# Kernel optimization log

Measured on AMD Instinct MI355X. Metric: run time of the kernel, lower is better.

Reference implementation:

```python
import jax, jax.numpy as jnp
import numpy as np

EPS = 1e-12  # tf.nn.l2_normalize epsilon


def setup_inputs() -> dict:
    key = jax.random.key(0)
    k1, k2, k3 = jax.random.split(key, 3)
    T, NC, FW = 16384, 2048, 100
    x = jax.random.normal(k1, (T, NC), dtype=jnp.float32)
    weights = jax.random.normal(k2, (FW, NC), dtype=jnp.float32)
    biases = jax.random.normal(k3, (1, NC), dtype=jnp.float32)
    return {"x": x, "weights": weights, "biases": biases}


def reference(x, weights, biases):
    # x: [T, NC] (batch_size is the time axis), weights: [FW, NC], biases: [1, NC]
    FW, NC = weights.shape
    # pos_constraint then L2-normalize each filter along the lag axis
    w = jnp.maximum(weights, 0.0)
    w = w * jax.lax.rsqrt(jnp.maximum(jnp.sum(w * w, axis=0, keepdims=True), EPS))
    # The original pads the filter with FW trailing zeros and runs a SAME conv2d
    # over a [NC, T, 1, 1] input, then takes diag_part to recover the per-channel
    # result. With kernel size 2*FW, SAME pads (FW-1) above / FW below; the FW
    # trailing zero taps never contribute, so this equals a cross-correlation
    # with left padding FW-1: out[t, c] = sum_k w[k, c] * x[t + k - (FW-1), c].
    xT = x.T[None]                 # [1, NC, T]
    kern = w.T[:, None, :]         # [NC, 1, FW] depthwise kernel (OIH)
    pre = jax.lax.conv_general_dilated(
        xT, kern,
        window_strides=(1,),
        padding=[(FW - 1, 0)],
        dimension_numbers=("NCH", "OIH", "NCH"),
        feature_group_count=NC,
    )                              # [1, NC, T]
    pre = pre[0].T + biases        # [T, NC]
    return pre  # activation_func='lin' -> identity
```

## Files before the change

### kernel.cpp

```cpp
#include <hip/hip_runtime.h>


#define T_TOT 16384
#define NCH   2048
#define FW    100
#define CB    32
#define TB    128
#define NTHR  256
#define ROWL  292
#define NSEG  8
#define NCHUNK (T_TOT / TB / NSEG)

#define KC_STEP(KI, PH, NS) do {                                                \
    int ro_ = (base0 + (KI)*8 + 16) & 255;                                      \
    float4 n0_ = *(const float4*)(rrow + ro_);                                  \
    float4 n1_ = *(const float4*)(rrow + ro_ + 4);                              \
    xw[(NS)+0]=n0_.x; xw[(NS)+1]=n0_.y; xw[(NS)+2]=n0_.z; xw[(NS)+3]=n0_.w;     \
    xw[(NS)+4]=n1_.x; xw[(NS)+5]=n1_.y; xw[(NS)+6]=n1_.z; xw[(NS)+7]=n1_.w;     \
    _Pragma("unroll")                                                           \
    for (int u_ = 0; u_ < 8; ++u_) {                                            \
      _Pragma("unroll")                                                         \
      for (int i_ = 0; i_ < 16; ++i_)                                           \
        acc[i_] = fmaf(wreg[(KI)*8 + u_], xw[((PH) + u_ + i_) % 24], acc[i_]);  \
    }                                                                           \
} while (0)

__global__ __launch_bounds__(NTHR, 2)
void catent_fir(const float* __restrict__ x,
                const float* __restrict__ wraw,
                const float* __restrict__ bias,
                float* __restrict__ out) {
    __shared__ __align__(16) float ring[CB * ROWL];

    const int tid   = threadIdx.x;
    const int cgrp  = blockIdx.x & 63;
    const int sidx  = blockIdx.x >> 6;
    const int cbase = cgrp * CB;

    const int ch0 = sidx * NCHUNK;
    const int tseg0 = ch0 * TB;

    const int c = tid & 31;
    const int g = tid >> 5;

    float wreg[104];
    {
        const float* wcol = wraw + cbase + c;
        float s = 0.0f;
        wreg[0] = 0.0f;
        #pragma unroll
        for (int j = 1; j <= FW; ++j) {
            float v = fmaxf(wcol[(size_t)(j - 1) * NCH], 0.0f);
            wreg[j] = v;
            s = fmaf(v, v, s);
        }
        wreg[101] = 0.0f; wreg[102] = 0.0f; wreg[103] = 0.0f;
        float scl = rsqrtf(fmaxf(s, 1e-12f));
        #pragma unroll
        for (int j = 1; j <= FW; ++j) wreg[j] *= scl;
    }

    {
        float* rw = &ring[c * ROWL];
        for (int p = 0; p < 2; ++p) {
            int tbase = tseg0 - TB + p * TB + g * 16;
            float v[16];
            #pragma unroll
            for (int j = 0; j < 16; ++j) {
                int t = tbase + j;
                v[j] = (t >= 0) ? x[(size_t)t * NCH + cbase + c] : 0.0f;
            }
            int rm = tbase & 255;
            #pragma unroll
            for (int q = 0; q < 4; ++q)
                *(float4*)(rw + rm + q * 4) = make_float4(v[q*4], v[q*4+1], v[q*4+2], v[q*4+3]);
            if (rm < 32) {
                #pragma unroll
                for (int q = 0; q < 4; ++q)
                    *(float4*)(rw + 256 + rm + q * 4) = make_float4(v[q*4], v[q*4+1], v[q*4+2], v[q*4+3]);
            }
        }
    }
    __syncthreads();

    const float biasr = bias[cbase + c];
    const float* rrow = &ring[c * ROWL];
    float* rwr = &ring[c * ROWL];

    for (int ch = ch0; ch < ch0 + NCHUNK; ++ch) {
        const int t0 = ch * TB;
        const bool do_stage = (ch + 1 < ch0 + NCHUNK);

        float stv[16];
        if (do_stage) {
            const size_t gb = (size_t)(t0 + TB + g * 16) * NCH + cbase + c;
            #pragma unroll
            for (int j = 0; j < 16; ++j) stv[j] = x[gb + (size_t)j * NCH];
        }

        float acc[16];
        #pragma unroll
        for (int i = 0; i < 16; ++i) acc[i] = biasr;

        float xw[24];
        const int base0 = t0 + g * 16 - 100;

        {
            int ro = base0 & 255;
            #pragma unroll
            for (int q = 0; q < 6; ++q) {
                float4 v = *(const float4*)(rrow + ro + q * 4);
                xw[q*4+0] = v.x; xw[q*4+1] = v.y; xw[q*4+2] = v.z; xw[q*4+3] = v.w;
            }
            #pragma unroll
            for (int u = 0; u < 8; ++u) {
                #pragma unroll
                for (int i = 0; i < 16; ++i)
                    acc[i] = fmaf(wreg[u], xw[(u + i) % 24], acc[i]);
            }
        }

        KC_STEP(1,  8, 0);
        KC_STEP(2, 16, 8);
        KC_STEP(3,  0, 16);
        KC_STEP(4,  8, 0);
        KC_STEP(5, 16, 8);
        KC_STEP(6,  0, 16);
        KC_STEP(7,  8, 0);
        KC_STEP(8, 16, 8);
        KC_STEP(9,  0, 16);
        KC_STEP(10, 8, 0);
        KC_STEP(11,16, 8);
        KC_STEP(12, 0, 16);

        __syncthreads();

        if (do_stage) {
            int rm = (t0 + TB + g * 16) & 255;
            #pragma unroll
            for (int q = 0; q < 4; ++q)
                *(float4*)(rwr + rm + q * 4) = make_float4(stv[q*4], stv[q*4+1], stv[q*4+2], stv[q*4+3]);
            if (rm < 32) {
                #pragma unroll
                for (int q = 0; q < 4; ++q)
                    *(float4*)(rwr + 256 + rm + q * 4) = make_float4(stv[q*4], stv[q*4+1], stv[q*4+2], stv[q*4+3]);
            }
        }
        __syncthreads();

        {
            size_t ob = (size_t)(t0 + g * 16) * NCH + cbase + c;
            #pragma unroll
            for (int i = 0; i < 16; ++i) out[ob + (size_t)i * NCH] = acc[i];
        }
    }
}

extern "C" void kernel_launch(void* const* d_in, const int* in_sizes, int n_in,
                              void* d_out, int out_size, void* d_ws, size_t ws_size,
                              hipStream_t stream) {
    const float* x    = (const float*)d_in[0];
    const float* wraw = (const float*)d_in[1];
    const float* bias = (const float*)d_in[2];
    float* out = (float*)d_out;

    dim3 grid(64 * NSEG);
    dim3 block(NTHR);
    catent_fir<<<grid, block, 0, stream>>>(x, wraw, bias, out);
}
```

Before: 107.1 us.

## Move normalized filter taps from registers to LDS to raise occupancy

The 104 per-thread weight registers are replaced by a per-channel weight table in shared memory, written by the first warp group and read back as float4 pairs inside each KC step. Launch bounds go from 2 to 3 blocks per SM, and the time axis is split into 12 uneven segments instead of 8 so the grid is larger. This aims to cut register pressure and raise occupancy and latency hiding, at the cost of extra LDS reads per chunk and more halo reloads across segments. There is no barrier between the LDS weight writes and the first reads, but the existing __syncthreads after ring staging already covers this.

Result: slower. 321.0 us (+199.8%).

```diff
diff --git a/kernel.cpp b/kernel.cpp
--- a/kernel.cpp
+++ b/kernel.cpp
@@ -8,56 +8,69 @@
 #define TB    128
 #define NTHR  256
 #define ROWL  292
-#define NSEG  8
-#define NCHUNK (T_TOT / TB / NSEG)
+#define WROW  108
+#define NSEG  12
+#define NCHUNK_TOT (T_TOT / TB)
 
 #define KC_STEP(KI, PH, NS) do {                                                \
     int ro_ = (base0 + (KI)*8 + 16) & 255;                                      \
     float4 n0_ = *(const float4*)(rrow + ro_);                                  \
     float4 n1_ = *(const float4*)(rrow + ro_ + 4);                              \
+    float4 w0_ = *(const float4*)(wrow + (KI)*8);                               \
+    float4 w1_ = *(const float4*)(wrow + (KI)*8 + 4);                           \
     xw[(NS)+0]=n0_.x; xw[(NS)+1]=n0_.y; xw[(NS)+2]=n0_.z; xw[(NS)+3]=n0_.w;     \
     xw[(NS)+4]=n1_.x; xw[(NS)+5]=n1_.y; xw[(NS)+6]=n1_.z; xw[(NS)+7]=n1_.w;     \
+    float wk_[8];                                                               \
+    wk_[0]=w0_.x; wk_[1]=w0_.y; wk_[2]=w0_.z; wk_[3]=w0_.w;                     \
+    wk_[4]=w1_.x; wk_[5]=w1_.y; wk_[6]=w1_.z; wk_[7]=w1_.w;                     \
     _Pragma("unroll")                                                           \
     for (int u_ = 0; u_ < 8; ++u_) {                                            \
       _Pragma("unroll")                                                         \
       for (int i_ = 0; i_ < 16; ++i_)                                           \
-        acc[i_] = fmaf(wreg[(KI)*8 + u_], xw[((PH) + u_ + i_) % 24], acc[i_]);  \
+        acc[i_] = fmaf(wk_[u_], xw[((PH) + u_ + i_) % 24], acc[i_]);            \
     }                                                                           \
 } while (0)
 
-__global__ __launch_bounds__(NTHR, 2)
+__global__ __launch_bounds__(NTHR, 3)
 void catent_fir(const float* __restrict__ x,
                 const float* __restrict__ wraw,
                 const float* __restrict__ bias,
                 float* __restrict__ out) {
     __shared__ __align__(16) float ring[CB * ROWL];
+    __shared__ __align__(16) float wl[CB * WROW];
 
     const int tid   = threadIdx.x;
     const int cgrp  = blockIdx.x & 63;
     const int sidx  = blockIdx.x >> 6;
     const int cbase = cgrp * CB;
 
-    const int ch0 = sidx * NCHUNK;
+    const int ch0 = (sidx * NCHUNK_TOT) / NSEG;
+    const int ch1 = ((sidx + 1) * NCHUNK_TOT) / NSEG;
     const int tseg0 = ch0 * TB;
 
     const int c = tid & 31;
     const int g = tid >> 5;
 
-    float wreg[104];
     {
         const float* wcol = wraw + cbase + c;
+        float wt[104];
         float s = 0.0f;
-        wreg[0] = 0.0f;
+        wt[0] = 0.0f;
         #pragma unroll
         for (int j = 1; j <= FW; ++j) {
             float v = fmaxf(wcol[(size_t)(j - 1) * NCH], 0.0f);
-            wreg[j] = v;
+            wt[j] = v;
             s = fmaf(v, v, s);
         }
-        wreg[101] = 0.0f; wreg[102] = 0.0f; wreg[103] = 0.0f;
+        wt[101] = 0.0f; wt[102] = 0.0f; wt[103] = 0.0f;
         float scl = rsqrtf(fmaxf(s, 1e-12f));
-        #pragma unroll
-        for (int j = 1; j <= FW; ++j) wreg[j] *= scl;
+        if (g == 0) {
+            float* wr = &wl[c * WROW];
+            #pragma unroll
+            for (int q = 0; q < 26; ++q)
+                *(float4*)(wr + q * 4) = make_float4(wt[q*4] * scl, wt[q*4+1] * scl,
+                                                    wt[q*4+2] * scl, wt[q*4+3] * scl);
+        }
     }
 
     {
@@ -85,11 +98,12 @@
 
     const float biasr = bias[cbase + c];
     const float* rrow = &ring[c * ROWL];
+    const float* wrow = &wl[c * WROW];
     float* rwr = &ring[c * ROWL];
 
-    for (int ch = ch0; ch < ch0 + NCHUNK; ++ch) {
+    for (int ch = ch0; ch < ch1; ++ch) {
         const int t0 = ch * TB;
-        const bool do_stage = (ch + 1 < ch0 + NCHUNK);
+        const bool do_stage = (ch + 1 < ch1);
 
         float stv[16];
         if (do_stage) {
@@ -112,11 +126,16 @@
                 float4 v = *(const float4*)(rrow + ro + q * 4);
                 xw[q*4+0] = v.x; xw[q*4+1] = v.y; xw[q*4+2] = v.z; xw[q*4+3] = v.w;
             }
+            float4 w0 = *(const float4*)(wrow);
+            float4 w1 = *(const float4*)(wrow + 4);
+            float wk[8];
+            wk[0]=w0.x; wk[1]=w0.y; wk[2]=w0.z; wk[3]=w0.w;
+            wk[4]=w1.x; wk[5]=w1.y; wk[6]=w1.z; wk[7]=w1.w;
             #pragma unroll
             for (int u = 0; u < 8; ++u) {
                 #pragma unroll
                 for (int i = 0; i < 16; ++i)
-                    acc[i] = fmaf(wreg[u], xw[(u + i) % 24], acc[i]);
+                    acc[i] = fmaf(wk[u], xw[(u + i) % 24], acc[i]);
             }
         }
 
```

## Precompute normalized weights in a prep kernel and stream them from global memory

Applied to the files above, without the earlier changes.

Adds a small prep kernel that applies the ReLU and L2 normalization and writes per-channel transposed weights into a global buffer. The main FIR kernel drops its 104-register weight array and instead loads 8 weights at a time via double-buffered float4 loads. The prefetch of the next x chunk is moved from before the compute to after the barrier, which cuts register pressure but removes the overlap between the global loads and the FMAs. The goals are lower VGPR usage and higher occupancy, at the cost of repeated weight loads from cache each chunk and a second kernel launch.

Result: slower. 123.6 us (+15.4%).

```diff
diff --git a/kernel.cpp b/kernel.cpp
--- a/kernel.cpp
+++ b/kernel.cpp
@@ -8,26 +8,51 @@
 #define TB    128
 #define NTHR  256
 #define ROWL  292
+#define WTL   104
 #define NSEG  8
 #define NCHUNK (T_TOT / TB / NSEG)
 
-#define KC_STEP(KI, PH, NS) do {                                                \
+__device__ float g_wT[NCH * WTL];
+
+__global__ void prep_w(const float* __restrict__ wraw) {
+    int c = blockIdx.x * 256 + threadIdx.x;
+    const float* wcol = wraw + c;
+    float s = 0.0f;
+    for (int k = 0; k < FW; ++k) {
+        float v = fmaxf(wcol[(size_t)k * NCH], 0.0f);
+        s = fmaf(v, v, s);
+    }
+    float scl = rsqrtf(fmaxf(s, 1e-12f));
+    float* wr = g_wT + (size_t)c * WTL;
+    wr[0] = 0.0f;
+    for (int j = 1; j <= FW; ++j)
+        wr[j] = fmaxf(wcol[(size_t)(j - 1) * NCH], 0.0f) * scl;
+    wr[101] = 0.0f; wr[102] = 0.0f; wr[103] = 0.0f;
+}
+
+#define KC_STEP(KI, PH, NS, WB0, WB1, DOLD, LDOFF) do {                         \
     int ro_ = (base0 + (KI)*8 + 16) & 255;                                      \
     float4 n0_ = *(const float4*)(rrow + ro_);                                  \
     float4 n1_ = *(const float4*)(rrow + ro_ + 4);                              \
+    float wk_[8];                                                               \
+    wk_[0]=WB0.x; wk_[1]=WB0.y; wk_[2]=WB0.z; wk_[3]=WB0.w;                     \
+    wk_[4]=WB1.x; wk_[5]=WB1.y; wk_[6]=WB1.z; wk_[7]=WB1.w;                     \
+    if (DOLD) {                                                                 \
+        WB0 = *(const float4*)(wrow + (LDOFF));                                 \
+        WB1 = *(const float4*)(wrow + (LDOFF) + 4);                             \
+    }                                                                           \
     xw[(NS)+0]=n0_.x; xw[(NS)+1]=n0_.y; xw[(NS)+2]=n0_.z; xw[(NS)+3]=n0_.w;     \
     xw[(NS)+4]=n1_.x; xw[(NS)+5]=n1_.y; xw[(NS)+6]=n1_.z; xw[(NS)+7]=n1_.w;     \
     _Pragma("unroll")                                                           \
     for (int u_ = 0; u_ < 8; ++u_) {                                            \
       _Pragma("unroll")                                                         \
       for (int i_ = 0; i_ < 16; ++i_)                                           \
-        acc[i_] = fmaf(wreg[(KI)*8 + u_], xw[((PH) + u_ + i_) % 24], acc[i_]);  \
+        acc[i_] = fmaf(wk_[u_], xw[((PH) + u_ + i_) % 24], acc[i_]);            \
     }                                                                           \
 } while (0)
 
 __global__ __launch_bounds__(NTHR, 2)
 void catent_fir(const float* __restrict__ x,
-                const float* __restrict__ wraw,
                 const float* __restrict__ bias,
                 float* __restrict__ out) {
     __shared__ __align__(16) float ring[CB * ROWL];
@@ -42,23 +67,6 @@
 
     const int c = tid & 31;
     const int g = tid >> 5;
-
-    float wreg[104];
-    {
-        const float* wcol = wraw + cbase + c;
-        float s = 0.0f;
-        wreg[0] = 0.0f;
-        #pragma unroll
-        for (int j = 1; j <= FW; ++j) {
-            float v = fmaxf(wcol[(size_t)(j - 1) * NCH], 0.0f);
-            wreg[j] = v;
-            s = fmaf(v, v, s);
-        }
-        wreg[101] = 0.0f; wreg[102] = 0.0f; wreg[103] = 0.0f;
-        float scl = rsqrtf(fmaxf(s, 1e-12f));
-        #pragma unroll
-        for (int j = 1; j <= FW; ++j) wreg[j] *= scl;
-    }
 
     {
         float* rw = &ring[c * ROWL];
@@ -85,18 +93,17 @@
 
     const float biasr = bias[cbase + c];
     const float* rrow = &ring[c * ROWL];
+    const float* wrow = g_wT + (size_t)(cbase + c) * WTL;
     float* rwr = &ring[c * ROWL];
 
     for (int ch = ch0; ch < ch0 + NCHUNK; ++ch) {
         const int t0 = ch * TB;
         const bool do_stage = (ch + 1 < ch0 + NCHUNK);
 
-        float stv[16];
-        if (do_stage) {
-            const size_t gb = (size_t)(t0 + TB + g * 16) * NCH + cbase + c;
-            #pragma unroll
-            for (int j = 0; j < 16; ++j) stv[j] = x[gb + (size_t)j * NCH];
-        }
+        float4 wA0 = *(const float4*)(wrow);
+        float4 wA1 = *(const float4*)(wrow + 4);
+        float4 wB0 = *(const float4*)(wrow + 8);
+        float4 wB1 = *(const float4*)(wrow + 12);
 
         float acc[16];
         #pragma unroll
@@ -112,38 +119,48 @@
                 float4 v = *(const float4*)(rrow + ro + q * 4);
                 xw[q*4+0] = v.x; xw[q*4+1] = v.y; xw[q*4+2] = v.z; xw[q*4+3] = v.w;
             }
+            float wk[8];
+            wk[0]=wA0.x; wk[1]=wA0.y; wk[2]=wA0.z; wk[3]=wA0.w;
+            wk[4]=wA1.x; wk[5]=wA1.y; wk[6]=wA1.z; wk[7]=wA1.w;
+            wA0 = *(const float4*)(wrow + 16);
+            wA1 = *(const float4*)(wrow + 20);
             #pragma unroll
             for (int u = 0; u < 8; ++u) {
                 #pragma unroll
                 for (int i = 0; i < 16; ++i)
-                    acc[i] = fmaf(wreg[u], xw[(u + i) % 24], acc[i]);
+                    acc[i] = fmaf(wk[u], xw[(u + i) % 24], acc[i]);
             }
         }
 
-        KC_STEP(1,  8, 0);
-        KC_STEP(2, 16, 8);
-        KC_STEP(3,  0, 16);
-        KC_STEP(4,  8, 0);
-        KC_STEP(5, 16, 8);
-        KC_STEP(6,  0, 16);
-        KC_STEP(7,  8, 0);
-        KC_STEP(8, 16, 8);
-        KC_STEP(9,  0, 16);
-        KC_STEP(10, 8, 0);
-        KC_STEP(11,16, 8);
-        KC_STEP(12, 0, 16);
+        KC_STEP(1,  8,  0, wB0, wB1, 1, 24);
+        KC_STEP(2, 16,  8, wA0, wA1, 1, 32);
+        KC_STEP(3,  0, 16, wB0, wB1, 1, 40);
+        KC_STEP(4,  8,  0, wA0, wA1, 1, 48);
+        KC_STEP(5, 16,  8, wB0, wB1, 1, 56);
+        KC_STEP(6,  0, 16, wA0, wA1, 1, 64);
+        KC_STEP(7,  8,  0, wB0, wB1, 1, 72);
+        KC_STEP(8, 16,  8, wA0, wA1, 1, 80);
+        KC_STEP(9,  0, 16, wB0, wB1, 1, 88);
+        KC_STEP(10, 8,  0, wA0, wA1, 1, 96);
+        KC_STEP(11,16,  8, wB0, wB1, 0, 0);
+        KC_STEP(12, 0, 16, wA0, wA1, 0, 0);
 
         __syncthreads();
 
         if (do_stage) {
-            int rm = (t0 + TB + g * 16) & 255;
+            const int tb = t0 + TB + g * 16;
+            const size_t gb = (size_t)tb * NCH + cbase + c;
+            float sv[16];
+            #pragma unroll
+            for (int j = 0; j < 16; ++j) sv[j] = x[gb + (size_t)j * NCH];
+            int rm = tb & 255;
             #pragma unroll
             for (int q = 0; q < 4; ++q)
-                *(float4*)(rwr + rm + q * 4) = make_float4(stv[q*4], stv[q*4+1], stv[q*4+2], stv[q*4+3]);
+                *(float4*)(rwr + rm + q * 4) = make_float4(sv[q*4], sv[q*4+1], sv[q*4+2], sv[q*4+3]);
             if (rm < 32) {
                 #pragma unroll
                 for (int q = 0; q < 4; ++q)
-                    *(float4*)(rwr + 256 + rm + q * 4) = make_float4(stv[q*4], stv[q*4+1], stv[q*4+2], stv[q*4+3]);
+                    *(float4*)(rwr + 256 + rm + q * 4) = make_float4(sv[q*4], sv[q*4+1], sv[q*4+2], sv[q*4+3]);
             }
         }
         __syncthreads();
@@ -164,7 +181,6 @@
     const float* bias = (const float*)d_in[2];
     float* out = (float*)d_out;
 
-    dim3 grid(64 * NSEG);
-    dim3 block(NTHR);
-    catent_fir<<<grid, block, 0, stream>>>(x, wraw, bias, out);
+    prep_w<<<dim3(NCH / 256), dim3(256), 0, stream>>>(wraw);
+    catent_fir<<<dim3(64 * NSEG), dim3(NTHR), 0, stream>>>(x, bias, out);
 }
```
